# Kernel optimization log

Hardware: AMD Instinct MI355X
Metric: run time of the kernel (lower is better)

## Reference

```python
import jax, jax.numpy as jnp
import numpy as np

NUM_HEADS = 16
EMBED_DIM = 1024
HEAD_DIM = EMBED_DIM // NUM_HEADS


def setup_inputs() -> dict:
    key = jax.random.key(0)
    kq, kk, kv, kw, kb = jax.random.split(key, 5)
    B, S, D = 2, 2048, EMBED_DIM
    bound = 1.0 / np.sqrt(D)
    return {
        "query": jax.random.normal(kq, (B, S, D), dtype=jnp.float32),
        "key": jax.random.normal(kk, (B, S, D), dtype=jnp.float32),
        "value": jax.random.normal(kv, (B, S, D), dtype=jnp.float32),
        "W_out": jax.random.uniform(kw, (D, D), minval=-bound, maxval=bound, dtype=jnp.float32),
        "b_out": jax.random.uniform(kb, (D,), minval=-bound, maxval=bound, dtype=jnp.float32),
        "prelu_a": jnp.array(0.25, dtype=jnp.float32),
    }


def reference(query, key, value, W_out, b_out, prelu_a):
    B, S, D = query.shape
    # Note: the original forward never applies q/k/v linear layers, only reshape.
    q = query.reshape(B, S, NUM_HEADS, HEAD_DIM)  # b s h d
    k = key.reshape(B, S, NUM_HEADS, HEAD_DIM)
    v = value.reshape(B, S, NUM_HEADS, HEAD_DIM)
    scale = 1.0 / np.sqrt(HEAD_DIM).astype(np.float32)
    scores = jnp.einsum("bqhd,bkhd->bhqk", q, k) * scale  # [B,H,S,S]
    attn = jax.nn.softmax(scores, axis=-1)
    out = jnp.einsum("bhqk,bkhd->bqhd", attn, v).reshape(B, S, D)
    out = out @ W_out.T + b_out  # torch Linear: x @ W.T + b
    # dropout is identity in eval mode; PReLU with single scalar param
    out = jnp.where(out >= 0, out, prelu_a * out)
    return out
```

## Files before the change

kernel.cpp:

```cpp
#include <hip/hip_runtime.h>
#include <hip/hip_bf16.h>

typedef __attribute__((ext_vector_type(8))) short bf16x8;
typedef __attribute__((ext_vector_type(4))) float f32x4;

#define S_LEN 2048
#define EMB   1024
#define NH    16
#define HD    64

__device__ inline int swz(int row, int chunk) {
  return row * 64 + ((chunk ^ (row & 7)) << 3);
}

__device__ inline int swz128(int row, int chunk) {
  return row * 128 + ((chunk ^ (row & 15)) << 3);
}

__device__ inline int kperm(int s) {
  return (s & 0x23) | ((s & 0x04) << 2) | ((s & 0x18) >> 1);
}

__device__ inline uint4 cvt8(const float* __restrict__ src, float scale) {
  float4 f0 = ((const float4*)src)[0];
  float4 f1 = ((const float4*)src)[1];
  __hip_bfloat16 t[8];
  t[0] = __float2bfloat16(f0.x * scale);
  t[1] = __float2bfloat16(f0.y * scale);
  t[2] = __float2bfloat16(f0.z * scale);
  t[3] = __float2bfloat16(f0.w * scale);
  t[4] = __float2bfloat16(f1.x * scale);
  t[5] = __float2bfloat16(f1.y * scale);
  t[6] = __float2bfloat16(f1.z * scale);
  t[7] = __float2bfloat16(f1.w * scale);
  return *(uint4*)t;
}

__global__ __launch_bounds__(256)
void prep(const float* __restrict__ K, const float* __restrict__ V,
          const float* __restrict__ W,
          __hip_bfloat16* __restrict__ Kb, __hip_bfloat16* __restrict__ Vt,
          __hip_bfloat16* __restrict__ Wb) {
  const int tid = threadIdx.x;
  if (blockIdx.z == 2) {
    const int widx = blockIdx.y * 32 + blockIdx.x;
    const int i = (widx * 256 + tid) * 8;
    *(uint4*)(Wb + i) = cvt8(W + i, 1.0f);
    return;
  }
  __shared__ float vt[64 * 65];
  const int st = blockIdx.x, h = blockIdx.y, b = blockIdx.z;
  const size_t srcbase = ((size_t)(b * S_LEN + st * 64)) * EMB + h * HD;
  const size_t kvb = ((size_t)(b * NH + h) * S_LEN + st * 64) * HD;
  const size_t vtb = ((size_t)(b * NH + h) * HD) * S_LEN + st * 64;

  for (int c = tid; c < 512; c += 256) {
    const int r = c >> 3, c8 = (c & 7) * 8;
    *(uint4*)(Kb + kvb + r * HD + c8) = cvt8(K + srcbase + (size_t)r * EMB + c8, 1.0f);
    const float* vsrc = V + srcbase + (size_t)r * EMB + c8;
    float4 a = ((const float4*)vsrc)[0];
    float4 d4 = ((const float4*)vsrc)[1];
    float tv[8] = {a.x, a.y, a.z, a.w, d4.x, d4.y, d4.z, d4.w};
    #pragma unroll
    for (int j = 0; j < 8; ++j) vt[r * 65 + c8 + j] = tv[j];
  }
  __syncthreads();
  for (int c = tid; c < 512; c += 256) {
    const int d = c >> 3, s8 = (c & 7) * 8;
    __hip_bfloat16 t[8];
    #pragma unroll
    for (int j = 0; j < 8; ++j)
      t[j] = __float2bfloat16(vt[(s8 + j) * 65 + d]);
    *(uint4*)(Vt + vtb + (size_t)d * S_LEN + s8) = *(uint4*)t;
  }
}

__global__ __launch_bounds__(512, 4)
void attn_fwd(const float* __restrict__ Q,
              const __hip_bfloat16* __restrict__ Kb,
              const __hip_bfloat16* __restrict__ Vt,
              __hip_bfloat16* __restrict__ O)
{
  __shared__ __align__(16) __hip_bfloat16 qs[128 * 64];
  __shared__ __align__(16) __hip_bfloat16 ks[2][128 * 64];
  __shared__ __align__(16) __hip_bfloat16 vs[2][64 * 128];

  const int qt   = blockIdx.x;
  const int h    = blockIdx.y;
  const int b    = blockIdx.z;
  const int tid  = threadIdx.x;
  const int wave = tid >> 6;
  const int lane = tid & 63;
  const int ln   = lane & 15;
  const int qd   = lane >> 4;

  const size_t baseQ = ((size_t)(b * S_LEN + qt * 128)) * EMB + h * HD;
  const size_t kvb   = ((size_t)(b * NH + h) * S_LEN) * HD;
  const size_t vtb   = ((size_t)(b * NH + h) * HD) * S_LEN;

  const int r0 = tid >> 3, cc = tid & 7;
  const int kpos0 = swz(kperm(r0), cc);
  const int kpos1 = kpos0 + 64 * 64;
  const int vr0 = tid >> 4, vch = tid & 15;
  const int vpos0 = swz128(vr0, vch);
  const int vpos1 = vpos0 + 32 * 128;

  uint4 kreg0 = *(const uint4*)(Kb + kvb + (size_t)(r0)       * HD + cc * 8);
  uint4 kreg1 = *(const uint4*)(Kb + kvb + (size_t)(64 + r0)  * HD + cc * 8);
  uint4 vreg0 = *(const uint4*)(Vt + vtb + (size_t)vr0        * S_LEN + vch * 8);
  uint4 vreg1 = *(const uint4*)(Vt + vtb + (size_t)(vr0 + 32) * S_LEN + vch * 8);

  const float qscale = 0.125f * 1.44269504088896f;
  #pragma unroll
  for (int i = 0; i < 2; ++i) {
    const int c = tid + 512 * i, row = c >> 3, ch = c & 7;
    *(uint4*)&qs[swz(row, ch)] = cvt8(Q + baseQ + (size_t)row * EMB + ch * 8, qscale);
  }
  *(uint4*)&ks[0][kpos0] = kreg0;
  *(uint4*)&ks[0][kpos1] = kreg1;
  *(uint4*)&vs[0][vpos0] = vreg0;
  *(uint4*)&vs[0][vpos1] = vreg1;
  kreg0 = *(const uint4*)(Kb + kvb + (size_t)(128 + r0)      * HD + cc * 8);
  kreg1 = *(const uint4*)(Kb + kvb + (size_t)(192 + r0)      * HD + cc * 8);
  vreg0 = *(const uint4*)(Vt + vtb + (size_t)vr0        * S_LEN + 128 + vch * 8);
  vreg1 = *(const uint4*)(Vt + vtb + (size_t)(vr0 + 32) * S_LEN + 128 + vch * 8);
  __syncthreads();

  bf16x8 aq[2];
  #pragma unroll
  for (int kh = 0; kh < 2; ++kh)
    aq[kh] = *(const bf16x8*)&qs[swz(wave * 16 + ln, kh * 4 + qd)];

  bf16x8 ones;
  #pragma unroll
  for (int j = 0; j < 8; ++j) ones[j] = (short)0x3F80;

  f32x4 oacc[4] = {};
  f32x4 lacc = {};

  for (int kt = 0; kt < S_LEN / 128; ++kt) {
    const int cur = kt & 1;
    if (kt + 1 < S_LEN / 128) {
      *(uint4*)&ks[1 - cur][kpos0] = kreg0;
      *(uint4*)&ks[1 - cur][kpos1] = kreg1;
      *(uint4*)&vs[1 - cur][vpos0] = vreg0;
      *(uint4*)&vs[1 - cur][vpos1] = vreg1;
      if (kt + 2 < S_LEN / 128) {
        const int kb2 = (kt + 2) * 128;
        kreg0 = *(const uint4*)(Kb + kvb + (size_t)(kb2 + r0)       * HD + cc * 8);
        kreg1 = *(const uint4*)(Kb + kvb + (size_t)(kb2 + 64 + r0)  * HD + cc * 8);
        vreg0 = *(const uint4*)(Vt + vtb + (size_t)vr0        * S_LEN + kb2 + vch * 8);
        vreg1 = *(const uint4*)(Vt + vtb + (size_t)(vr0 + 32) * S_LEN + kb2 + vch * 8);
      }
    }

    f32x4 sfA[4], sfB[4];
    __builtin_amdgcn_s_setprio(1);
    #pragma unroll
    for (int k16 = 0; k16 < 4; ++k16) {
      const int krow = k16 * 16 + ln;
      bf16x8 ak0 = *(const bf16x8*)&ks[cur][swz(krow, qd)];
      bf16x8 ak1 = *(const bf16x8*)&ks[cur][swz(krow, 4 + qd)];
      f32x4 acc = {};
      acc = __builtin_amdgcn_mfma_f32_16x16x32_bf16(ak0, aq[0], acc, 0, 0, 0);
      sfA[k16] = __builtin_amdgcn_mfma_f32_16x16x32_bf16(ak1, aq[1], acc, 0, 0, 0);
    }
    #pragma unroll
    for (int k16 = 0; k16 < 4; ++k16) {
      const int krow = (4 + k16) * 16 + ln;
      bf16x8 ak0 = *(const bf16x8*)&ks[cur][swz(krow, qd)];
      bf16x8 ak1 = *(const bf16x8*)&ks[cur][swz(krow, 4 + qd)];
      f32x4 acc = {};
      acc = __builtin_amdgcn_mfma_f32_16x16x32_bf16(ak0, aq[0], acc, 0, 0, 0);
      sfB[k16] = __builtin_amdgcn_mfma_f32_16x16x32_bf16(ak1, aq[1], acc, 0, 0, 0);
    }
    __builtin_amdgcn_s_setprio(0);

    bf16x8 apA[2];
    #pragma unroll
    for (int t2 = 0; t2 < 2; ++t2)
      #pragma unroll
      for (int j = 0; j < 8; ++j) {
        const float p = __builtin_amdgcn_exp2f(sfA[t2 * 2 + (j >> 2)][j & 3]);
        __hip_bfloat16 hb = __float2bfloat16(p);
        apA[t2][j] = *(short*)&hb;
      }

    __builtin_amdgcn_s_setprio(1);
    #pragma unroll
    for (int t = 0; t < 2; ++t) {
      lacc = __builtin_amdgcn_mfma_f32_16x16x32_bf16(apA[t], ones, lacc, 0, 0, 0);
      #pragma unroll
      for (int dn = 0; dn < 4; ++dn) {
        bf16x8 bv = *(const bf16x8*)&vs[cur][swz128(dn * 16 + ln, t * 4 + qd)];
        oacc[dn] = __builtin_amdgcn_mfma_f32_16x16x32_bf16(apA[t], bv, oacc[dn], 0, 0, 0);
      }
    }
    __builtin_amdgcn_s_setprio(0);

    bf16x8 apB[2];
    #pragma unroll
    for (int t2 = 0; t2 < 2; ++t2)
      #pragma unroll
      for (int j = 0; j < 8; ++j) {
        const float p = __builtin_amdgcn_exp2f(sfB[t2 * 2 + (j >> 2)][j & 3]);
        __hip_bfloat16 hb = __float2bfloat16(p);
        apB[t2][j] = *(short*)&hb;
      }

    __builtin_amdgcn_s_setprio(1);
    #pragma unroll
    for (int t = 0; t < 2; ++t) {
      lacc = __builtin_amdgcn_mfma_f32_16x16x32_bf16(apB[t], ones, lacc, 0, 0, 0);
      #pragma unroll
      for (int dn = 0; dn < 4; ++dn) {
        bf16x8 bv = *(const bf16x8*)&vs[cur][swz128(dn * 16 + ln, (2 + t) * 4 + qd)];
        oacc[dn] = __builtin_amdgcn_mfma_f32_16x16x32_bf16(apB[t], bv, oacc[dn], 0, 0, 0);
      }
    }
    __builtin_amdgcn_s_setprio(0);

    __syncthreads();
  }

  #pragma unroll
  for (int r = 0; r < 4; ++r) {
    const float inv = 1.f / lacc[r];
    const int row = wave * 16 + qd * 4 + r;
    #pragma unroll
    for (int dn = 0; dn < 4; ++dn)
      O[baseQ + (size_t)row * EMB + dn * 16 + ln] =
          __float2bfloat16(oacc[dn][r] * inv);
  }
}

__global__ __launch_bounds__(256, 2)
void proj_prelu(const __hip_bfloat16* __restrict__ X,
                const __hip_bfloat16* __restrict__ Wb,
                const float* __restrict__ Bv,
                const float* __restrict__ Pa,
                float* __restrict__ Out)
{
  __shared__ __align__(16) __hip_bfloat16 xs[2][128 * 64];
  __shared__ __align__(16) __hip_bfloat16 wsm[2][64 * 64];

  const int m0   = blockIdx.x * 128;
  const int n0   = blockIdx.y * 64;
  const int tid  = threadIdx.x;
  const int wave = tid >> 6;
  const int wm   = wave >> 1;
  const int wn   = wave & 1;
  const int lane = tid & 63;
  const int ln   = lane & 15;
  const int qd   = lane >> 4;

  const int r0 = tid >> 3, cc = tid & 7;

  f32x4 acc[8] = {};

  uint4 xg0, xg1, xg2, xg3, wg0, wg1;
  #define LOADK(ko)                                                           \
    xg0 = *(const uint4*)(X  + (size_t)(m0 + r0     ) * EMB + (ko) + cc * 8); \
    xg1 = *(const uint4*)(X  + (size_t)(m0 + r0 + 32) * EMB + (ko) + cc * 8); \
    xg2 = *(const uint4*)(X  + (size_t)(m0 + r0 + 64) * EMB + (ko) + cc * 8); \
    xg3 = *(const uint4*)(X  + (size_t)(m0 + r0 + 96) * EMB + (ko) + cc * 8); \
    wg0 = *(const uint4*)(Wb + (size_t)(n0 + r0     ) * EMB + (ko) + cc * 8); \
    wg1 = *(const uint4*)(Wb + (size_t)(n0 + r0 + 32) * EMB + (ko) + cc * 8)
  #define STORELDS(buf)                                                       \
    *(uint4*)&xs [buf][swz(r0,      cc)] = xg0;                               \
    *(uint4*)&xs [buf][swz(r0 + 32, cc)] = xg1;                               \
    *(uint4*)&xs [buf][swz(r0 + 64, cc)] = xg2;                               \
    *(uint4*)&xs [buf][swz(r0 + 96, cc)] = xg3;                               \
    *(uint4*)&wsm[buf][swz(r0,      cc)] = wg0;                               \
    *(uint4*)&wsm[buf][swz(r0 + 32, cc)] = wg1

  LOADK(0);
  STORELDS(0);
  LOADK(64);
  __syncthreads();

  for (int kt = 0; kt < EMB / 64; ++kt) {
    const int cur = kt & 1;
    if (kt + 1 < EMB / 64) {
      STORELDS(1 - cur);
      if (kt + 2 < EMB / 64) {
        LOADK((kt + 2) * 64);
      }
    }

    #pragma unroll
    for (int ks2 = 0; ks2 < 2; ++ks2) {
      bf16x8 ax0 = *(const bf16x8*)&xs[cur][swz(wm * 64 +  0 + ln, ks2 * 4 + qd)];
      bf16x8 ax1 = *(const bf16x8*)&xs[cur][swz(wm * 64 + 16 + ln, ks2 * 4 + qd)];
      bf16x8 ax2 = *(const bf16x8*)&xs[cur][swz(wm * 64 + 32 + ln, ks2 * 4 + qd)];
      bf16x8 ax3 = *(const bf16x8*)&xs[cur][swz(wm * 64 + 48 + ln, ks2 * 4 + qd)];
      bf16x8 bw0 = *(const bf16x8*)&wsm[cur][swz(wn * 32 +  0 + ln, ks2 * 4 + qd)];
      bf16x8 bw1 = *(const bf16x8*)&wsm[cur][swz(wn * 32 + 16 + ln, ks2 * 4 + qd)];
      acc[0] = __builtin_amdgcn_mfma_f32_16x16x32_bf16(ax0, bw0, acc[0], 0, 0, 0);
      acc[1] = __builtin_amdgcn_mfma_f32_16x16x32_bf16(ax0, bw1, acc[1], 0, 0, 0);
      acc[2] = __builtin_amdgcn_mfma_f32_16x16x32_bf16(ax1, bw0, acc[2], 0, 0, 0);
      acc[3] = __builtin_amdgcn_mfma_f32_16x16x32_bf16(ax1, bw1, acc[3], 0, 0, 0);
      acc[4] = __builtin_amdgcn_mfma_f32_16x16x32_bf16(ax2, bw0, acc[4], 0, 0, 0);
      acc[5] = __builtin_amdgcn_mfma_f32_16x16x32_bf16(ax2, bw1, acc[5], 0, 0, 0);
      acc[6] = __builtin_amdgcn_mfma_f32_16x16x32_bf16(ax3, bw0, acc[6], 0, 0, 0);
      acc[7] = __builtin_amdgcn_mfma_f32_16x16x32_bf16(ax3, bw1, acc[7], 0, 0, 0);
    }
    __syncthreads();
  }

  const float a = Pa[0];
  #pragma unroll
  for (int mf = 0; mf < 4; ++mf) {
    #pragma unroll
    for (int nf = 0; nf < 2; ++nf) {
      const float bn = Bv[n0 + wn * 32 + nf * 16 + ln];
      #pragma unroll
      for (int r = 0; r < 4; ++r) {
        float y = acc[mf * 2 + nf][r] + bn;
        y = (y >= 0.f) ? y : a * y;
        Out[(size_t)(m0 + wm * 64 + mf * 16 + qd * 4 + r) * EMB +
            n0 + wn * 32 + nf * 16 + ln] = y;
      }
    }
  }
  #undef LOADK
  #undef STORELDS
}

extern "C" void kernel_launch(void* const* d_in, const int* in_sizes, int n_in,
                              void* d_out, int out_size, void* d_ws, size_t ws_size,
                              hipStream_t stream) {
  const float* Q  = (const float*)d_in[0];
  const float* K  = (const float*)d_in[1];
  const float* V  = (const float*)d_in[2];
  const float* W  = (const float*)d_in[3];
  const float* Bb = (const float*)d_in[4];
  const float* Pa = (const float*)d_in[5];
  float* Out = (float*)d_out;

  char* ws = (char*)d_ws;
  __hip_bfloat16* Xws = (__hip_bfloat16*)(ws);
  __hip_bfloat16* Kb  = (__hip_bfloat16*)(ws + (8u  << 20));
  __hip_bfloat16* Vt  = (__hip_bfloat16*)(ws + (16u << 20));
  __hip_bfloat16* Wb  = (__hip_bfloat16*)(ws + (24u << 20));

  prep      <<<dim3(S_LEN / 64, NH, 3), 256, 0, stream>>>(K, V, W, Kb, Vt, Wb);
  attn_fwd  <<<dim3(S_LEN / 128, NH, 2), 512, 0, stream>>>(Q, Kb, Vt, Xws);
  proj_prelu<<<dim3(2 * S_LEN / 128, EMB / 64), 256, 0, stream>>>(Xws, Wb, Bb, Pa, Out);
}
```

Baseline: 153.4 us.

## Split-K the output projection into two partial GEMMs plus a reduce kernel

The output projection GEMM is split along K into two halves run as separate blocks via grid z, each writing fp32 partials to workspace buffers. A new elementwise kernel then sums the partials, adds the bias and applies PReLU. This doubles the block count (from 512) to improve CU occupancy and load balance on a small-M GEMM. In exchange it adds an extra kernel launch and about 32 MB of fp32 partial writes and reads. The original fused kernel is kept as a fallback when the workspace is too small.

Measured after the change: 161.2 us. +5.1%, slower.

```diff
diff --git a/kernel.cpp b/kernel.cpp
--- a/kernel.cpp
+++ b/kernel.cpp
@@ -234,18 +234,19 @@
   }
 }
 
-__global__ __launch_bounds__(256, 2)
-void proj_prelu(const __hip_bfloat16* __restrict__ X,
-                const __hip_bfloat16* __restrict__ Wb,
-                const float* __restrict__ Bv,
-                const float* __restrict__ Pa,
-                float* __restrict__ Out)
+__global__ __launch_bounds__(256, 3)
+void proj_gemm(const __hip_bfloat16* __restrict__ X,
+               const __hip_bfloat16* __restrict__ Wb,
+               float* __restrict__ P0,
+               float* __restrict__ P1)
 {
   __shared__ __align__(16) __hip_bfloat16 xs[2][128 * 64];
   __shared__ __align__(16) __hip_bfloat16 wsm[2][64 * 64];
 
   const int m0   = blockIdx.x * 128;
   const int n0   = blockIdx.y * 64;
+  const int kb0  = blockIdx.z * 512;
+  float* __restrict__ P = blockIdx.z ? P1 : P0;
   const int tid  = threadIdx.x;
   const int wave = tid >> 6;
   const int wm   = wave >> 1;
@@ -274,17 +275,17 @@
     *(uint4*)&wsm[buf][swz(r0,      cc)] = wg0;                               \
     *(uint4*)&wsm[buf][swz(r0 + 32, cc)] = wg1
 
-  LOADK(0);
+  LOADK(kb0);
   STORELDS(0);
-  LOADK(64);
+  LOADK(kb0 + 64);
   __syncthreads();
 
-  for (int kt = 0; kt < EMB / 64; ++kt) {
+  for (int kt = 0; kt < 8; ++kt) {
     const int cur = kt & 1;
-    if (kt + 1 < EMB / 64) {
+    if (kt + 1 < 8) {
       STORELDS(1 - cur);
-      if (kt + 2 < EMB / 64) {
-        LOADK((kt + 2) * 64);
+      if (kt + 2 < 8) {
+        LOADK(kb0 + (kt + 2) * 64);
       }
     }
 
@@ -308,6 +309,111 @@
     __syncthreads();
   }
 
+  #pragma unroll
+  for (int mf = 0; mf < 4; ++mf)
+    #pragma unroll
+    for (int nf = 0; nf < 2; ++nf)
+      #pragma unroll
+      for (int r = 0; r < 4; ++r)
+        P[(size_t)(m0 + wm * 64 + mf * 16 + qd * 4 + r) * EMB +
+          n0 + wn * 32 + nf * 16 + ln] = acc[mf * 2 + nf][r];
+  #undef LOADK
+  #undef STORELDS
+}
+
+__global__ __launch_bounds__(256)
+void proj_reduce(const float* __restrict__ P0, const float* __restrict__ P1,
+                 const float* __restrict__ Bv, const float* __restrict__ Pa,
+                 float* __restrict__ Out)
+{
+  const float a = Pa[0];
+  const size_t i = ((size_t)blockIdx.x * 256 + threadIdx.x) * 8;
+  const int col = (int)(i & (EMB - 1));
+  float4 x0 = ((const float4*)(P0 + i))[0], x1 = ((const float4*)(P0 + i))[1];
+  float4 y0 = ((const float4*)(P1 + i))[0], y1 = ((const float4*)(P1 + i))[1];
+  float4 b0 = ((const float4*)(Bv + col))[0], b1 = ((const float4*)(Bv + col))[1];
+  float v[8] = {x0.x + y0.x + b0.x, x0.y + y0.y + b0.y,
+                x0.z + y0.z + b0.z, x0.w + y0.w + b0.w,
+                x1.x + y1.x + b1.x, x1.y + y1.y + b1.y,
+                x1.z + y1.z + b1.z, x1.w + y1.w + b1.w};
+  #pragma unroll
+  for (int j = 0; j < 8; ++j) v[j] = (v[j] >= 0.f) ? v[j] : a * v[j];
+  ((float4*)(Out + i))[0] = *(float4*)&v[0];
+  ((float4*)(Out + i))[1] = *(float4*)&v[4];
+}
+
+__global__ __launch_bounds__(256, 2)
+void proj_prelu(const __hip_bfloat16* __restrict__ X,
+                const __hip_bfloat16* __restrict__ Wb,
+                const float* __restrict__ Bv,
+                const float* __restrict__ Pa,
+                float* __restrict__ Out)
+{
+  __shared__ __align__(16) __hip_bfloat16 xs[2][128 * 64];
+  __shared__ __align__(16) __hip_bfloat16 wsm[2][64 * 64];
+
+  const int m0   = blockIdx.x * 128;
+  const int n0   = blockIdx.y * 64;
+  const int tid  = threadIdx.x;
+  const int wave = tid >> 6;
+  const int wm   = wave >> 1;
+  const int wn   = wave & 1;
+  const int lane = tid & 63;
+  const int ln   = lane & 15;
+  const int qd   = lane >> 4;
+  const int r0 = tid >> 3, cc = tid & 7;
+
+  f32x4 acc[8] = {};
+
+  uint4 xg0, xg1, xg2, xg3, wg0, wg1;
+  #define LOADK(ko)                                                           \
+    xg0 = *(const uint4*)(X  + (size_t)(m0 + r0     ) * EMB + (ko) + cc * 8); \
+    xg1 = *(const uint4*)(X  + (size_t)(m0 + r0 + 32) * EMB + (ko) + cc * 8); \
+    xg2 = *(const uint4*)(X  + (size_t)(m0 + r0 + 64) * EMB + (ko) + cc * 8); \
+    xg3 = *(const uint4*)(X  + (size_t)(m0 + r0 + 96) * EMB + (ko) + cc * 8); \
+    wg0 = *(const uint4*)(Wb + (size_t)(n0 + r0     ) * EMB + (ko) + cc * 8); \
+    wg1 = *(const uint4*)(Wb + (size_t)(n0 + r0 + 32) * EMB + (ko) + cc * 8)
+  #define STORELDS(buf)                                                       \
+    *(uint4*)&xs [buf][swz(r0,      cc)] = xg0;                               \
+    *(uint4*)&xs [buf][swz(r0 + 32, cc)] = xg1;                               \
+    *(uint4*)&xs [buf][swz(r0 + 64, cc)] = xg2;                               \
+    *(uint4*)&xs [buf][swz(r0 + 96, cc)] = xg3;                               \
+    *(uint4*)&wsm[buf][swz(r0,      cc)] = wg0;                               \
+    *(uint4*)&wsm[buf][swz(r0 + 32, cc)] = wg1
+
+  LOADK(0);
+  STORELDS(0);
+  LOADK(64);
+  __syncthreads();
+
+  for (int kt = 0; kt < EMB / 64; ++kt) {
+    const int cur = kt & 1;
+    if (kt + 1 < EMB / 64) {
+      STORELDS(1 - cur);
+      if (kt + 2 < EMB / 64) {
+        LOADK((kt + 2) * 64);
+      }
+    }
+    #pragma unroll
+    for (int ks2 = 0; ks2 < 2; ++ks2) {
+      bf16x8 ax0 = *(const bf16x8*)&xs[cur][swz(wm * 64 +  0 + ln, ks2 * 4 + qd)];
+      bf16x8 ax1 = *(const bf16x8*)&xs[cur][swz(wm * 64 + 16 + ln, ks2 * 4 + qd)];
+      bf16x8 ax2 = *(const bf16x8*)&xs[cur][swz(wm * 64 + 32 + ln, ks2 * 4 + qd)];
+      bf16x8 ax3 = *(const bf16x8*)&xs[cur][swz(wm * 64 + 48 + ln, ks2 * 4 + qd)];
+      bf16x8 bw0 = *(const bf16x8*)&wsm[cur][swz(wn * 32 +  0 + ln, ks2 * 4 + qd)];
+      bf16x8 bw1 = *(const bf16x8*)&wsm[cur][swz(wn * 32 + 16 + ln, ks2 * 4 + qd)];
+      acc[0] = __builtin_amdgcn_mfma_f32_16x16x32_bf16(ax0, bw0, acc[0], 0, 0, 0);
+      acc[1] = __builtin_amdgcn_mfma_f32_16x16x32_bf16(ax0, bw1, acc[1], 0, 0, 0);
+      acc[2] = __builtin_amdgcn_mfma_f32_16x16x32_bf16(ax1, bw0, acc[2], 0, 0, 0);
+      acc[3] = __builtin_amdgcn_mfma_f32_16x16x32_bf16(ax1, bw1, acc[3], 0, 0, 0);
+      acc[4] = __builtin_amdgcn_mfma_f32_16x16x32_bf16(ax2, bw0, acc[4], 0, 0, 0);
+      acc[5] = __builtin_amdgcn_mfma_f32_16x16x32_bf16(ax2, bw1, acc[5], 0, 0, 0);
+      acc[6] = __builtin_amdgcn_mfma_f32_16x16x32_bf16(ax3, bw0, acc[6], 0, 0, 0);
+      acc[7] = __builtin_amdgcn_mfma_f32_16x16x32_bf16(ax3, bw1, acc[7], 0, 0, 0);
+    }
+    __syncthreads();
+  }
+
   const float a = Pa[0];
   #pragma unroll
   for (int mf = 0; mf < 4; ++mf) {
@@ -346,5 +452,13 @@
 
   prep      <<<dim3(S_LEN / 64, NH, 3), 256, 0, stream>>>(K, V, W, Kb, Vt, Wb);
   attn_fwd  <<<dim3(S_LEN / 128, NH, 2), 512, 0, stream>>>(Q, Kb, Vt, Xws);
-  proj_prelu<<<dim3(2 * S_LEN / 128, EMB / 64), 256, 0, stream>>>(Xws, Wb, Bb, Pa, Out);
-}
+
+  if (ws_size >= (64ull << 20)) {
+    float* P0 = (float*)(ws + (28ull << 20));
+    float* P1 = (float*)(ws + (46ull << 20));
+    proj_gemm  <<<dim3(2 * S_LEN / 128, EMB / 64, 2), 256, 0, stream>>>(Xws, Wb, P0, P1);
+    proj_reduce<<<2 * S_LEN * EMB / (256 * 8), 256, 0, stream>>>(P0, P1, Bb, Pa, Out);
+  } else {
+    proj_prelu <<<dim3(2 * S_LEN / 128, EMB / 64), 256, 0, stream>>>(Xws, Wb, Bb, Pa, Out);
+  }
+}
```

## Fuse K and W bf16 conversion into attention and projection loads

Applied to the files above, without the earlier changes.

Stops pre-converting K and W to bf16 in the prep kernel. The attention kernel now reads fp32 K straight from the strided input and converts it to bf16 while writing to LDS, and the projection kernel does the same for W. This removes a workspace write and read pass for K and W and makes the prep kernel smaller. In exchange, the hot loops issue twice as many global load bytes for K and W, hold more registers, and repeat the conversion for every query tile (K) and every M tile (W).

After: 156.2 us. About the same (+1.8%).

```diff
diff --git a/kernel.cpp b/kernel.cpp
--- a/kernel.cpp
+++ b/kernel.cpp
@@ -36,27 +36,34 @@
   return *(uint4*)t;
 }
 
+__device__ inline uint4 cvt8r(float4 f0, float4 f1) {
+  __hip_bfloat16 t[8];
+  t[0] = __float2bfloat16(f0.x);
+  t[1] = __float2bfloat16(f0.y);
+  t[2] = __float2bfloat16(f0.z);
+  t[3] = __float2bfloat16(f0.w);
+  t[4] = __float2bfloat16(f1.x);
+  t[5] = __float2bfloat16(f1.y);
+  t[6] = __float2bfloat16(f1.z);
+  t[7] = __float2bfloat16(f1.w);
+  return *(uint4*)t;
+}
+
+__device__ inline void ld8f(const float* __restrict__ p, float4& a, float4& b) {
+  a = ((const float4*)p)[0];
+  b = ((const float4*)p)[1];
+}
+
 __global__ __launch_bounds__(256)
-void prep(const float* __restrict__ K, const float* __restrict__ V,
-          const float* __restrict__ W,
-          __hip_bfloat16* __restrict__ Kb, __hip_bfloat16* __restrict__ Vt,
-          __hip_bfloat16* __restrict__ Wb) {
+void prep(const float* __restrict__ V, __hip_bfloat16* __restrict__ Vt) {
+  __shared__ float vt[64 * 65];
   const int tid = threadIdx.x;
-  if (blockIdx.z == 2) {
-    const int widx = blockIdx.y * 32 + blockIdx.x;
-    const int i = (widx * 256 + tid) * 8;
-    *(uint4*)(Wb + i) = cvt8(W + i, 1.0f);
-    return;
-  }
-  __shared__ float vt[64 * 65];
   const int st = blockIdx.x, h = blockIdx.y, b = blockIdx.z;
   const size_t srcbase = ((size_t)(b * S_LEN + st * 64)) * EMB + h * HD;
-  const size_t kvb = ((size_t)(b * NH + h) * S_LEN + st * 64) * HD;
   const size_t vtb = ((size_t)(b * NH + h) * HD) * S_LEN + st * 64;
 
   for (int c = tid; c < 512; c += 256) {
     const int r = c >> 3, c8 = (c & 7) * 8;
-    *(uint4*)(Kb + kvb + r * HD + c8) = cvt8(K + srcbase + (size_t)r * EMB + c8, 1.0f);
     const float* vsrc = V + srcbase + (size_t)r * EMB + c8;
     float4 a = ((const float4*)vsrc)[0];
     float4 d4 = ((const float4*)vsrc)[1];
@@ -77,7 +84,7 @@
 
 __global__ __launch_bounds__(512, 4)
 void attn_fwd(const float* __restrict__ Q,
-              const __hip_bfloat16* __restrict__ Kb,
+              const float* __restrict__ K,
               const __hip_bfloat16* __restrict__ Vt,
               __hip_bfloat16* __restrict__ O)
 {
@@ -95,7 +102,7 @@
   const int qd   = lane >> 4;
 
   const size_t baseQ = ((size_t)(b * S_LEN + qt * 128)) * EMB + h * HD;
-  const size_t kvb   = ((size_t)(b * NH + h) * S_LEN) * HD;
+  const size_t baseK = ((size_t)(b * S_LEN)) * EMB + h * HD;
   const size_t vtb   = ((size_t)(b * NH + h) * HD) * S_LEN;
 
   const int r0 = tid >> 3, cc = tid & 7;
@@ -105,8 +112,9 @@
   const int vpos0 = swz128(vr0, vch);
   const int vpos1 = vpos0 + 32 * 128;
 
-  uint4 kreg0 = *(const uint4*)(Kb + kvb + (size_t)(r0)       * HD + cc * 8);
-  uint4 kreg1 = *(const uint4*)(Kb + kvb + (size_t)(64 + r0)  * HD + cc * 8);
+  float4 ka0, kb0, ka1, kb1;
+  ld8f(K + baseK + (size_t)(r0)      * EMB + cc * 8, ka0, kb0);
+  ld8f(K + baseK + (size_t)(64 + r0) * EMB + cc * 8, ka1, kb1);
   uint4 vreg0 = *(const uint4*)(Vt + vtb + (size_t)vr0        * S_LEN + vch * 8);
   uint4 vreg1 = *(const uint4*)(Vt + vtb + (size_t)(vr0 + 32) * S_LEN + vch * 8);
 
@@ -116,12 +124,12 @@
     const int c = tid + 512 * i, row = c >> 3, ch = c & 7;
     *(uint4*)&qs[swz(row, ch)] = cvt8(Q + baseQ + (size_t)row * EMB + ch * 8, qscale);
   }
-  *(uint4*)&ks[0][kpos0] = kreg0;
-  *(uint4*)&ks[0][kpos1] = kreg1;
+  *(uint4*)&ks[0][kpos0] = cvt8r(ka0, kb0);
+  *(uint4*)&ks[0][kpos1] = cvt8r(ka1, kb1);
   *(uint4*)&vs[0][vpos0] = vreg0;
   *(uint4*)&vs[0][vpos1] = vreg1;
-  kreg0 = *(const uint4*)(Kb + kvb + (size_t)(128 + r0)      * HD + cc * 8);
-  kreg1 = *(const uint4*)(Kb + kvb + (size_t)(192 + r0)      * HD + cc * 8);
+  ld8f(K + baseK + (size_t)(128 + r0) * EMB + cc * 8, ka0, kb0);
+  ld8f(K + baseK + (size_t)(192 + r0) * EMB + cc * 8, ka1, kb1);
   vreg0 = *(const uint4*)(Vt + vtb + (size_t)vr0        * S_LEN + 128 + vch * 8);
   vreg1 = *(const uint4*)(Vt + vtb + (size_t)(vr0 + 32) * S_LEN + 128 + vch * 8);
   __syncthreads();
@@ -141,14 +149,14 @@
   for (int kt = 0; kt < S_LEN / 128; ++kt) {
     const int cur = kt & 1;
     if (kt + 1 < S_LEN / 128) {
-      *(uint4*)&ks[1 - cur][kpos0] = kreg0;
-      *(uint4*)&ks[1 - cur][kpos1] = kreg1;
+      *(uint4*)&ks[1 - cur][kpos0] = cvt8r(ka0, kb0);
+      *(uint4*)&ks[1 - cur][kpos1] = cvt8r(ka1, kb1);
       *(uint4*)&vs[1 - cur][vpos0] = vreg0;
       *(uint4*)&vs[1 - cur][vpos1] = vreg1;
       if (kt + 2 < S_LEN / 128) {
         const int kb2 = (kt + 2) * 128;
-        kreg0 = *(const uint4*)(Kb + kvb + (size_t)(kb2 + r0)       * HD + cc * 8);
-        kreg1 = *(const uint4*)(Kb + kvb + (size_t)(kb2 + 64 + r0)  * HD + cc * 8);
+        ld8f(K + baseK + (size_t)(kb2 + r0)      * EMB + cc * 8, ka0, kb0);
+        ld8f(K + baseK + (size_t)(kb2 + 64 + r0) * EMB + cc * 8, ka1, kb1);
         vreg0 = *(const uint4*)(Vt + vtb + (size_t)vr0        * S_LEN + kb2 + vch * 8);
         vreg1 = *(const uint4*)(Vt + vtb + (size_t)(vr0 + 32) * S_LEN + kb2 + vch * 8);
       }
@@ -236,7 +244,7 @@
 
 __global__ __launch_bounds__(256, 2)
 void proj_prelu(const __hip_bfloat16* __restrict__ X,
-                const __hip_bfloat16* __restrict__ Wb,
+                const float* __restrict__ W,
                 const float* __restrict__ Bv,
                 const float* __restrict__ Pa,
                 float* __restrict__ Out)
@@ -258,21 +266,22 @@
 
   f32x4 acc[8] = {};
 
-  uint4 xg0, xg1, xg2, xg3, wg0, wg1;
+  uint4 xg0, xg1, xg2, xg3;
+  float4 wa0, wb0, wa1, wb1;
   #define LOADK(ko)                                                           \
     xg0 = *(const uint4*)(X  + (size_t)(m0 + r0     ) * EMB + (ko) + cc * 8); \
     xg1 = *(const uint4*)(X  + (size_t)(m0 + r0 + 32) * EMB + (ko) + cc * 8); \
     xg2 = *(const uint4*)(X  + (size_t)(m0 + r0 + 64) * EMB + (ko) + cc * 8); \
     xg3 = *(const uint4*)(X  + (size_t)(m0 + r0 + 96) * EMB + (ko) + cc * 8); \
-    wg0 = *(const uint4*)(Wb + (size_t)(n0 + r0     ) * EMB + (ko) + cc * 8); \
-    wg1 = *(const uint4*)(Wb + (size_t)(n0 + r0 + 32) * EMB + (ko) + cc * 8)
+    ld8f(W + (size_t)(n0 + r0     ) * EMB + (ko) + cc * 8, wa0, wb0);         \
+    ld8f(W + (size_t)(n0 + r0 + 32) * EMB + (ko) + cc * 8, wa1, wb1)
   #define STORELDS(buf)                                                       \
     *(uint4*)&xs [buf][swz(r0,      cc)] = xg0;                               \
     *(uint4*)&xs [buf][swz(r0 + 32, cc)] = xg1;                               \
     *(uint4*)&xs [buf][swz(r0 + 64, cc)] = xg2;                               \
     *(uint4*)&xs [buf][swz(r0 + 96, cc)] = xg3;                               \
-    *(uint4*)&wsm[buf][swz(r0,      cc)] = wg0;                               \
-    *(uint4*)&wsm[buf][swz(r0 + 32, cc)] = wg1
+    *(uint4*)&wsm[buf][swz(r0,      cc)] = cvt8r(wa0, wb0);                   \
+    *(uint4*)&wsm[buf][swz(r0 + 32, cc)] = cvt8r(wa1, wb1)
 
   LOADK(0);
   STORELDS(0);
@@ -340,11 +349,9 @@
 
   char* ws = (char*)d_ws;
   __hip_bfloat16* Xws = (__hip_bfloat16*)(ws);
-  __hip_bfloat16* Kb  = (__hip_bfloat16*)(ws + (8u  << 20));
   __hip_bfloat16* Vt  = (__hip_bfloat16*)(ws + (16u << 20));
-  __hip_bfloat16* Wb  = (__hip_bfloat16*)(ws + (24u << 20));
-
-  prep      <<<dim3(S_LEN / 64, NH, 3), 256, 0, stream>>>(K, V, W, Kb, Vt, Wb);
-  attn_fwd  <<<dim3(S_LEN / 128, NH, 2), 512, 0, stream>>>(Q, Kb, Vt, Xws);
-  proj_prelu<<<dim3(2 * S_LEN / 128, EMB / 64), 256, 0, stream>>>(Xws, Wb, Bb, Pa, Out);
-}
+
+  prep      <<<dim3(S_LEN / 64, NH, 2), 256, 0, stream>>>(V, Vt);
+  attn_fwd  <<<dim3(S_LEN / 128, NH, 2), 512, 0, stream>>>(Q, K, Vt, Xws);
+  proj_prelu<<<dim3(2 * S_LEN / 128, EMB / 64), 256, 0, stream>>>(Xws, W, Bb, Pa, Out);
+}
```
